# Optimization experiments

Hardware: AMD Instinct MI355X
Metric: run time of the kernel (lower is better)

Reference implementation:

```python
import jax, jax.numpy as jnp
import numpy as np

N_NODES = 20000
N_EDGES = 480000
HIDDEN = 128
EDGE_FEAT = 128
BN_EPS = 1e-5


def setup_inputs() -> dict:
    key = jax.random.key(0)
    ks = jax.random.split(key, 6)
    z_dim = 2 * HIDDEN + EDGE_FEAT
    h = jax.random.normal(ks[0], (N_NODES, HIDDEN), dtype=jnp.float32)
    e = jax.random.normal(ks[1], (N_EDGES, EDGE_FEAT), dtype=jnp.float32)
    src = jax.random.randint(ks[2], (N_EDGES,), 0, N_NODES, dtype=jnp.int32)
    dst = jax.random.randint(ks[3], (N_EDGES,), 0, N_NODES, dtype=jnp.int32)
    W = jax.random.normal(ks[4], (z_dim, 2 * HIDDEN), dtype=jnp.float32) / np.sqrt(z_dim)
    b = jax.random.normal(ks[5], (2 * HIDDEN,), dtype=jnp.float32) * 0.01
    gamma = jnp.ones((2 * HIDDEN,), dtype=jnp.float32)
    beta = jnp.zeros((2 * HIDDEN,), dtype=jnp.float32)
    return {"h": h, "e": e, "src": src, "dst": dst, "W": W, "b": b,
            "gamma": gamma, "beta": beta}


def reference(h, e, src, dst, W, b, gamma, beta):
    # Gather endpoint features per edge: z = [h_src, h_dst, e]  -> [E, z_dim]
    z = jnp.concatenate([h[src], h[dst], e], axis=1)
    # Linear
    z = z @ W + b  # [E, 2*HIDDEN]
    # BatchNorm1d over the edge batch (training-mode stats, biased variance)
    mean = jnp.mean(z, axis=0)
    var = jnp.mean(jnp.square(z - mean), axis=0)
    z = (z - mean) * jax.lax.rsqrt(var + BN_EPS) * gamma + beta
    # Gated softplus message
    nbr_filter, nbr_core = jnp.split(z, 2, axis=1)
    msg = jax.nn.sigmoid(nbr_filter) * jax.nn.softplus(nbr_core)  # [E, HIDDEN]
    # Segment-sum reduce into destination nodes
    agg = jax.ops.segment_sum(msg, dst, num_segments=N_NODES)  # [N, HIDDEN]
    # Residual + softplus (dropout=0.0)
    return jax.nn.softplus(h + agg)
```

## Files before the change

kernel.cpp:

```cpp
#include <hip/hip_runtime.h>
#include <hip/hip_bf16.h>
#include <math.h>

#define N_NODES 20000
#define N_EDGES 480000
#define HIDDEN  128
#define ZDIM    384
#define NOUT    256
#define BN_EPS  1e-5f

#define LDA     392
#define LDZ     264

using bf16x8 = __attribute__((ext_vector_type(8))) short;
using f32x4  = __attribute__((ext_vector_type(4))) float;
using f32x16 = __attribute__((ext_vector_type(16))) float;
using s16x4  = __attribute__((ext_vector_type(4))) short;

struct f32x8 { float4 a, b; };

__device__ __forceinline__ unsigned short f2b(float f) {
    union { float f; unsigned u; } v; v.f = f;
    unsigned r = v.u + 0x7fffu + ((v.u >> 16) & 1u);
    return (unsigned short)(r >> 16);
}
__device__ __forceinline__ float bflo(unsigned u) {
    union { unsigned x; float f; } v; v.x = u << 16; return v.f;
}
__device__ __forceinline__ float bfhi(unsigned u) {
    union { unsigned x; float f; } v; v.x = u & 0xffff0000u; return v.f;
}
__device__ __forceinline__ float b2f(unsigned short s) {
    union { unsigned u; float f; } v; v.u = ((unsigned)s) << 16; return v.f;
}
__device__ __forceinline__ float sigmoid_(float x) {
    return 1.f / (1.f + __expf(-x));
}
__device__ __forceinline__ float softplus_(float x) {
    return fmaxf(x, 0.f) + __logf(1.f + __expf(-fabsf(x)));
}
__device__ __forceinline__ f32x8 ld8(const float* p) {
    f32x8 r; r.a = *(const float4*)p; r.b = *(const float4*)(p + 4); return r;
}
__device__ __forceinline__ bf16x8 cvt8(f32x8 v) {
    bf16x8 pk;
    pk[0] = (short)f2b(v.a.x); pk[1] = (short)f2b(v.a.y);
    pk[2] = (short)f2b(v.a.z); pk[3] = (short)f2b(v.a.w);
    pk[4] = (short)f2b(v.b.x); pk[5] = (short)f2b(v.b.y);
    pk[6] = (short)f2b(v.b.z); pk[7] = (short)f2b(v.b.w);
    return pk;
}

__global__ void convW(const float* __restrict__ W, short* __restrict__ wt) {
    int n = blockIdx.x;
    for (int k = threadIdx.x; k < ZDIM; k += 256)
        wt[n * ZDIM + k] = (short)f2b(W[(size_t)k * NOUT + n]);
}

__global__ void bn_finalize(const float* __restrict__ stats,
                            const float* __restrict__ gamma,
                            const float* __restrict__ beta,
                            float* __restrict__ scaleC,
                            float* __restrict__ shiftC) {
    int c = threadIdx.x;
    float s = 0.f, q = 0.f;
    for (int p = 0; p < 64; ++p) {
        s += stats[p * 512 + c];
        q += stats[p * 512 + 256 + c];
    }
    const float invE = 1.f / (float)N_EDGES;
    float m   = s * invE;
    float var = q * invE - m * m;
    float inv = rsqrtf(var + BN_EPS);
    float sc  = gamma[c] * inv;
    scaleC[c] = sc;
    shiftC[c] = beta[c] - m * sc;
}

__global__ void hist_dst(const int* __restrict__ dst, int* __restrict__ counts) {
    int i = blockIdx.x * 256 + threadIdx.x;
    if (i < N_EDGES) atomicAdd(&counts[dst[i]], 1);
}

__global__ void scan_nodes(const int* __restrict__ counts, int* __restrict__ offs,
                           int* __restrict__ cursor) {
    __shared__ int part[1024];
    int t = threadIdx.x;
    int base = t * 20;
    int local[20]; int s = 0;
    #pragma unroll
    for (int k = 0; k < 20; ++k) {
        int idx = base + k;
        int v = (idx < N_NODES) ? counts[idx] : 0;
        local[k] = s; s += v;
    }
    part[t] = s; __syncthreads();
    for (int d = 1; d < 1024; d <<= 1) {
        int v = (t >= d) ? part[t - d] : 0;
        __syncthreads();
        part[t] += v;
        __syncthreads();
    }
    int pre = (t > 0) ? part[t - 1] : 0;
    #pragma unroll
    for (int k = 0; k < 20; ++k) {
        int idx = base + k;
        if (idx < N_NODES) { int o = pre + local[k]; offs[idx] = o; cursor[idx] = o; }
    }
}

__global__ void build_ipos(const int* __restrict__ dst, int* __restrict__ cursor,
                           int* __restrict__ ipos) {
    int i = blockIdx.x * 256 + threadIdx.x;
    if (i < N_EDGES) ipos[i] = atomicAdd(&cursor[dst[i]], 1);
}

__global__ __launch_bounds__(256)
void node_proj(const float* __restrict__ h, const short* __restrict__ wt,
               unsigned short* __restrict__ P1, unsigned short* __restrict__ P2) {
    const int tid  = threadIdx.x;
    const int lane = tid & 63;
    const int l31  = lane & 31;
    const int hi   = lane >> 5;
    const int w    = tid >> 6;
    const int rowBase = blockIdx.x * 64;
    const int colBase = blockIdx.y * 256 + w * 64;

    const float* pA[2];
    #pragma unroll
    for (int mi = 0; mi < 2; ++mi) {
        int row = rowBase + mi * 32 + l31;
        if (row > N_NODES - 1) row = N_NODES - 1;
        pA[mi] = h + (size_t)row * HIDDEN + hi * 8;
    }
    const short* pB[2];
    #pragma unroll
    for (int n = 0; n < 2; ++n) {
        int c = colBase + n * 32 + l31;
        pB[n] = wt + (size_t)(c & 255) * ZDIM + (c >> 8) * 128 + hi * 8;
    }

    f32x16 acc[2][2] = {};
    #pragma unroll
    for (int kk = 0; kk < 8; ++kk) {
        bf16x8 a[2], b[2];
        #pragma unroll
        for (int mi = 0; mi < 2; ++mi) a[mi] = cvt8(ld8(pA[mi] + kk * 16));
        #pragma unroll
        for (int n = 0; n < 2; ++n) b[n] = *(const bf16x8*)(pB[n] + kk * 16);
        #pragma unroll
        for (int mi = 0; mi < 2; ++mi)
            #pragma unroll
            for (int n = 0; n < 2; ++n)
                acc[mi][n] = __builtin_amdgcn_mfma_f32_32x32x16_bf16(
                                 a[mi], b[n], acc[mi][n], 0, 0, 0);
    }

    unsigned short* Pt = (blockIdx.y == 0) ? P1 : P2;
    const int pcol = (w * 64) + l31 * 2;
    #pragma unroll
    for (int mi = 0; mi < 2; ++mi)
        #pragma unroll
        for (int r = 0; r < 16; ++r) {
            int row = rowBase + mi * 32 + 4 * hi + (r & 3) + 8 * (r >> 2);
            if (row < N_NODES) {
                unsigned pk = (unsigned)f2b(acc[mi][0][r]) |
                              ((unsigned)f2b(acc[mi][1][r]) << 16);
                *(unsigned*)&Pt[(size_t)row * 256 + pcol] = pk;
            }
        }
}

__global__ __launch_bounds__(256, 2)
void edge_gemm3(const float* __restrict__ e, const int* __restrict__ src,
                const int* __restrict__ dst, const short* __restrict__ wt,
                const int* __restrict__ ipos,
                const unsigned short* __restrict__ P1,
                const unsigned short* __restrict__ P2,
                float* __restrict__ stats, short* __restrict__ zout) {
    const int tid  = threadIdx.x;
    const int lane = tid & 63;
    const int l31  = lane & 31;
    const int hi   = lane >> 5;
    const int w    = tid >> 6;
    const int rowBase = blockIdx.x * 64;
    const int colBase = w * 64;
    const int pcol = colBase + l31 * 2;

    const float* pE[2];
    #pragma unroll
    for (int mi = 0; mi < 2; ++mi)
        pE[mi] = e + (size_t)(rowBase + mi * 32 + l31) * HIDDEN + hi * 8;
    const short* pB[2];
    #pragma unroll
    for (int n = 0; n < 2; ++n)
        pB[n] = wt + (size_t)(colBase + n * 32 + l31) * ZDIM + 256 + hi * 8;

    f32x8 t[2][4];
    #pragma unroll
    for (int mi = 0; mi < 2; ++mi)
        #pragma unroll
        for (int j = 0; j < 4; ++j) t[mi][j] = ld8(pE[mi] + j * 16);
    bf16x8 B[2][8];
    #pragma unroll
    for (int n = 0; n < 2; ++n)
        #pragma unroll
        for (int kk = 0; kk < 8; ++kk)
            B[n][kk] = *(const bf16x8*)(pB[n] + kk * 16);

    bf16x8 A0[2][4], A1[2][4];
    #pragma unroll
    for (int mi = 0; mi < 2; ++mi)
        #pragma unroll
        for (int j = 0; j < 4; ++j) A0[mi][j] = cvt8(t[mi][j]);
    #pragma unroll
    for (int mi = 0; mi < 2; ++mi)
        #pragma unroll
        for (int j = 0; j < 4; ++j) t[mi][j] = ld8(pE[mi] + 64 + j * 16);

    f32x16 acc[2][2] = {};
    #pragma unroll
    for (int kk = 0; kk < 4; ++kk)
        #pragma unroll
        for (int mi = 0; mi < 2; ++mi)
            #pragma unroll
            for (int n = 0; n < 2; ++n)
                acc[mi][n] = __builtin_amdgcn_mfma_f32_32x32x16_bf16(
                                 A0[mi][kk], B[n][kk], acc[mi][n], 0, 0, 0);
    #pragma unroll
    for (int mi = 0; mi < 2; ++mi)
        #pragma unroll
        for (int j = 0; j < 4; ++j) A1[mi][j] = cvt8(t[mi][j]);
    #pragma unroll
    for (int kk = 4; kk < 8; ++kk)
        #pragma unroll
        for (int mi = 0; mi < 2; ++mi)
            #pragma unroll
            for (int n = 0; n < 2; ++n)
                acc[mi][n] = __builtin_amdgcn_mfma_f32_32x32x16_bf16(
                                 A1[mi][kk - 4], B[n][kk], acc[mi][n], 0, 0, 0);

    unsigned ps[2][16], pd[2][16];
    int slot[2][16];
    #pragma unroll
    for (int mi = 0; mi < 2; ++mi)
        #pragma unroll
        for (int r = 0; r < 16; ++r) {
            int rowL = mi * 32 + 4 * hi + (r & 3) + 8 * (r >> 2);
            int g    = rowBase + rowL;
            int sI   = src[g];
            int dI   = dst[g];
            slot[mi][r] = ipos[g];
            ps[mi][r] = *(const unsigned*)&P1[(size_t)sI * 256 + pcol];
            pd[mi][r] = *(const unsigned*)&P2[(size_t)dI * 256 + pcol];
        }

    float s2[2] = {0.f, 0.f}, q2[2] = {0.f, 0.f};
    #pragma unroll
    for (int mi = 0; mi < 2; ++mi)
        #pragma unroll
        for (int r = 0; r < 16; ++r) {
            float z0 = acc[mi][0][r] + bflo(ps[mi][r]) + bflo(pd[mi][r]);
            float z1 = acc[mi][1][r] + bfhi(ps[mi][r]) + bfhi(pd[mi][r]);
            s2[0] += z0; q2[0] += z0 * z0;
            s2[1] += z1; q2[1] += z1 * z1;
            unsigned pk = (unsigned)f2b(z0) | ((unsigned)f2b(z1) << 16);
            *(unsigned*)&zout[(size_t)slot[mi][r] * NOUT + pcol] = pk;
        }
    float* base = stats + (size_t)(blockIdx.x & 63) * 512;
    #pragma unroll
    for (int n = 0; n < 2; ++n) {
        float s = s2[n], q = q2[n];
        s += __shfl_xor(s, 32, 64);
        q += __shfl_xor(q, 32, 64);
        if (lane < 32) {
            int col = colBase + n * 32 + l31;
            atomicAdd(base + col, s);
            atomicAdd(base + 256 + col, q);
        }
    }
}

template<int MODE>
__global__ __launch_bounds__(256)
void edge_gemm_fb(const float* __restrict__ h, const float* __restrict__ e,
                  const int* __restrict__ src, const int* __restrict__ dst,
                  const short* __restrict__ wt,
                  float* __restrict__ stats,
                  const float* __restrict__ scaleC, const float* __restrict__ shiftC,
                  float* __restrict__ agg) {
    const int tid  = threadIdx.x;
    const int bm   = blockIdx.x;
    const int rowBase = bm * 64;
    const int lane = tid & 63;
    const int brow = lane & 15;
    const int kgo  = (lane >> 4) * 8;
    const int wcol = (tid >> 6) * 64;

    __shared__ __align__(16) short lds[64 * LDA];

    #pragma unroll
    for (int j = 0; j < 12; ++j) {
        int u = tid + j * 256;
        int r = u / 48;
        int f0 = (u - r * 48) * 8;
        int row = rowBase + r;
        const float* p;
        if (f0 < 128)      p = h + (size_t)src[row] * HIDDEN + f0;
        else if (f0 < 256) p = h + (size_t)dst[row] * HIDDEN + (f0 - 128);
        else               p = e + (size_t)row * HIDDEN + (f0 - 256);
        *(bf16x8*)&lds[r * LDA + f0] = cvt8(ld8(p));
    }
    __syncthreads();

    const short* wB[4];
    #pragma unroll
    for (int n = 0; n < 4; ++n)
        wB[n] = wt + (size_t)(wcol + n * 16 + brow) * ZDIM + kgo;

    f32x4 acc[4][4] = {};
    #pragma unroll
    for (int kk = 0; kk < 12; ++kk) {
        bf16x8 aC[4], bC[4];
        #pragma unroll
        for (int m = 0; m < 4; ++m)
            aC[m] = *(const bf16x8*)&lds[(m * 16 + brow) * LDA + kk * 32 + kgo];
        #pragma unroll
        for (int n = 0; n < 4; ++n) bC[n] = *(const bf16x8*)(wB[n] + kk * 32);
        #pragma unroll
        for (int m = 0; m < 4; ++m)
            #pragma unroll
            for (int n = 0; n < 4; ++n)
                acc[m][n] = __builtin_amdgcn_mfma_f32_16x16x32_bf16(
                                aC[m], bC[n], acc[m][n], 0, 0, 0);
    }

    if (MODE == 1) {
        float* base = stats + (size_t)(bm & 63) * 512;
        #pragma unroll
        for (int n = 0; n < 4; ++n) {
            float s = 0.f, q = 0.f;
            #pragma unroll
            for (int m = 0; m < 4; ++m)
                #pragma unroll
                for (int r = 0; r < 4; ++r) {
                    float v = acc[m][n][r]; s += v; q += v * v;
                }
            s += __shfl_xor(s, 16, 64); s += __shfl_xor(s, 32, 64);
            q += __shfl_xor(q, 16, 64); q += __shfl_xor(q, 32, 64);
            if (lane < 16) {
                int col = wcol + n * 16 + lane;
                atomicAdd(base + col, s);
                atomicAdd(base + 256 + col, q);
            }
        }
    } else {
        float sc[4], sh[4];
        #pragma unroll
        for (int n = 0; n < 4; ++n) {
            int col = wcol + n * 16 + brow;
            sc[n] = scaleC[col]; sh[n] = shiftC[col];
        }
        __syncthreads();
        #pragma unroll
        for (int m = 0; m < 4; ++m) {
            int rowb = m * 16 + (lane >> 4) * 4;
            #pragma unroll
            for (int n = 0; n < 4; ++n) {
                int col = wcol + n * 16 + brow;
                #pragma unroll
                for (int r = 0; r < 4; ++r)
                    lds[(rowb + r) * LDZ + col] = (short)f2b(acc[m][n][r] * sc[n] + sh[n]);
            }
        }
        __syncthreads();
        const int c0 = (tid & 31) * 4;
        const int r0 = tid >> 5;
        #pragma unroll
        for (int rp = 0; rp < 8; ++rp) {
            int row = rp * 8 + r0;
            int d   = dst[rowBase + row];
            float* ap = agg + (size_t)d * HIDDEN + c0;
            s16x4 f4 = *(const s16x4*)&lds[row * LDZ + c0];
            s16x4 c4 = *(const s16x4*)&lds[row * LDZ + 128 + c0];
            #pragma unroll
            for (int j = 0; j < 4; ++j)
                atomicAdd(ap + j, sigmoid_(b2f((unsigned short)f4[j])) *
                                  softplus_(b2f((unsigned short)c4[j])));
        }
    }
}

__global__ __launch_bounds__(256)
void node_gather(const short* __restrict__ z,
                 const int* __restrict__ offs, const int* __restrict__ counts,
                 const float* __restrict__ scaleC, const float* __restrict__ shiftC,
                 const float* __restrict__ h, float* __restrict__ out) {
    int node = blockIdx.x * 4 + (threadIdx.x >> 6);
    int lane = threadIdx.x & 63;
    int l32  = lane & 31;
    const int wq = l32 >> 4;
    const int c0 = 64 * wq + 2 * (l32 & 15);

    float scF[4], shF[4], scS[4], shS[4];
    const int cmap[4] = {c0, c0 + 32, c0 + 1, c0 + 33};
    #pragma unroll
    for (int k = 0; k < 4; ++k) {
        scF[k] = scaleC[cmap[k]];       shF[k] = shiftC[cmap[k]];
        scS[k] = scaleC[128 + cmap[k]]; shS[k] = shiftC[128 + cmap[k]];
    }

    int s   = offs[node];
    int deg = counts[node];
    float a0 = 0.f, a1 = 0.f, a2 = 0.f, a3 = 0.f;
    const int po = 4 * l32;

    for (int j = (lane >> 5); j < deg; j += 4) {
        int jB = j + 2;
        bool hasB = (jB < deg);
        const short* zA = z + (size_t)(s + j) * NOUT;
        const short* zB = z + (size_t)(s + (hasB ? jB : j)) * NOUT;
        uint2 fA = *(const uint2*)(zA + po);
        uint2 cA = *(const uint2*)(zA + 128 + po);
        uint2 fB = *(const uint2*)(zB + po);
        uint2 cB = *(const uint2*)(zB + 128 + po);

        float f0 = bflo(fA.x) * scF[0] + shF[0];
        float f1 = bfhi(fA.x) * scF[1] + shF[1];
        float f2 = bflo(fA.y) * scF[2] + shF[2];
        float f3 = bfhi(fA.y) * scF[3] + shF[3];
        float g0 = bflo(cA.x) * scS[0] + shS[0];
        float g1 = bfhi(cA.x) * scS[1] + shS[1];
        float g2 = bflo(cA.y) * scS[2] + shS[2];
        float g3 = bfhi(cA.y) * scS[3] + shS[3];
        a0 += sigmoid_(f0) * softplus_(g0);
        a1 += sigmoid_(f1) * softplus_(g1);
        a2 += sigmoid_(f2) * softplus_(g2);
        a3 += sigmoid_(f3) * softplus_(g3);

        if (hasB) {
            f0 = bflo(fB.x) * scF[0] + shF[0];
            f1 = bfhi(fB.x) * scF[1] + shF[1];
            f2 = bflo(fB.y) * scF[2] + shF[2];
            f3 = bfhi(fB.y) * scF[3] + shF[3];
            g0 = bflo(cB.x) * scS[0] + shS[0];
            g1 = bfhi(cB.x) * scS[1] + shS[1];
            g2 = bflo(cB.y) * scS[2] + shS[2];
            g3 = bfhi(cB.y) * scS[3] + shS[3];
            a0 += sigmoid_(f0) * softplus_(g0);
            a1 += sigmoid_(f1) * softplus_(g1);
            a2 += sigmoid_(f2) * softplus_(g2);
            a3 += sigmoid_(f3) * softplus_(g3);
        }
    }
    a0 += __shfl_xor(a0, 32, 64);
    a1 += __shfl_xor(a1, 32, 64);
    a2 += __shfl_xor(a2, 32, 64);
    a3 += __shfl_xor(a3, 32, 64);

    if (lane < 32) {
        size_t o = (size_t)node * HIDDEN;
        float2 hA = *(const float2*)&h[o + c0];
        float2 hB = *(const float2*)&h[o + c0 + 32];
        float2 rA, rB;
        rA.x = softplus_(hA.x + a0);
        rA.y = softplus_(hA.y + a2);
        rB.x = softplus_(hB.x + a1);
        rB.y = softplus_(hB.y + a3);
        *(float2*)&out[o + c0]      = rA;
        *(float2*)&out[o + c0 + 32] = rB;
    }
}

__global__ void node_finalize(const float* __restrict__ h, float* __restrict__ out) {
    int i = blockIdx.x * 256 + threadIdx.x;
    float4 hv = ((const float4*)h)[i];
    float4 av = ((float4*)out)[i];
    float4 r;
    r.x = softplus_(hv.x + av.x);
    r.y = softplus_(hv.y + av.y);
    r.z = softplus_(hv.z + av.z);
    r.w = softplus_(hv.w + av.w);
    ((float4*)out)[i] = r;
}

extern "C" void kernel_launch(void* const* d_in, const int* in_sizes, int n_in,
                              void* d_out, int out_size, void* d_ws, size_t ws_size,
                              hipStream_t stream) {
    const float* h     = (const float*)d_in[0];
    const float* e     = (const float*)d_in[1];
    const int*   srcp  = (const int*)d_in[2];
    const int*   dstp  = (const int*)d_in[3];
    const float* W     = (const float*)d_in[4];
    const float* gamma = (const float*)d_in[6];
    const float* beta  = (const float*)d_in[7];
    float* out = (float*)d_out;

    char*  ws     = (char*)d_ws;
    float* stats  = (float*)ws;
    float* scaleC = (float*)(ws + 131072);
    float* shiftC = (float*)(ws + 132096);
    short* wt     = (short*)(ws + 133120);
    int*   counts = (int*)(ws + 329728);
    int*   offs   = (int*)(ws + 409856);
    int*   cursor = (int*)(ws + 489984);
    int*   ipos   = (int*)(ws + 570112);
    unsigned short* P1 = (unsigned short*)(ws + 2490112);
    unsigned short* P2 = (unsigned short*)(ws + 12730112);
    short* zbuf   = (short*)(ws + 22970112);
    const size_t need = 22970112ull + (size_t)N_EDGES * NOUT * 2;

    hipMemsetAsync(stats, 0, 131072, stream);
    convW<<<NOUT, 256, 0, stream>>>(W, wt);

    if (ws_size >= need) {
        hipMemsetAsync(counts, 0, N_NODES * sizeof(int), stream);
        hist_dst<<<(N_EDGES + 255) / 256, 256, 0, stream>>>(dstp, counts);
        scan_nodes<<<1, 1024, 0, stream>>>(counts, offs, cursor);
        build_ipos<<<(N_EDGES + 255) / 256, 256, 0, stream>>>(dstp, cursor, ipos);

        node_proj<<<dim3((N_NODES + 63) / 64, 2), 256, 0, stream>>>(h, wt, P1, P2);
        edge_gemm3<<<N_EDGES / 64, 256, 0, stream>>>(e, srcp, dstp, wt, ipos,
                P1, P2, stats, zbuf);
        bn_finalize<<<1, 256, 0, stream>>>(stats, gamma, beta, scaleC, shiftC);
        node_gather<<<N_NODES / 4, 256, 0, stream>>>(zbuf, offs, counts,
                scaleC, shiftC, h, out);
    } else {
        hipMemsetAsync(out, 0, (size_t)N_NODES * HIDDEN * sizeof(float), stream);
        edge_gemm_fb<1><<<N_EDGES / 64, 256, 0, stream>>>(h, e, srcp, dstp, wt,
                stats, nullptr, nullptr, nullptr);
        bn_finalize<<<1, 256, 0, stream>>>(stats, gamma, beta, scaleC, shiftC);
        edge_gemm_fb<2><<<N_EDGES / 64, 256, 0, stream>>>(h, e, srcp, dstp, wt,
                stats, scaleC, shiftC, out);
        node_finalize<<<N_NODES * HIDDEN / (4 * 256), 256, 0, stream>>>(h, out);
    }
}
```

Measured before the change: 472.7 us.

## Pack per-edge src/dst/slot into int4, raise edge GEMM occupancy, unroll gather by 4

The build pass now writes a packed int4 record (src, dst, slot) per edge, so the edge GEMM does one 16-byte load per row where it used to do three scattered int loads. The edge GEMM launch bound goes from 2 to 3 blocks per SM to raise occupancy, which may force register spills. The node gather loop handles four edges per iteration per half-wave, putting more loads in flight to hide memory latency. The trade is extra workspace and write traffic for the int4 array, plus more register pressure.

Result: slower. 621.3 us (+31.4%).

```diff
diff --git a/kernel.cpp b/kernel.cpp
--- a/kernel.cpp
+++ b/kernel.cpp
@@ -109,10 +109,14 @@
     }
 }
 
-__global__ void build_ipos(const int* __restrict__ dst, int* __restrict__ cursor,
-                           int* __restrict__ ipos) {
+__global__ void build_einfo(const int* __restrict__ src, const int* __restrict__ dst,
+                            int* __restrict__ cursor, int4* __restrict__ einfo) {
     int i = blockIdx.x * 256 + threadIdx.x;
-    if (i < N_EDGES) ipos[i] = atomicAdd(&cursor[dst[i]], 1);
+    if (i < N_EDGES) {
+        int d = dst[i];
+        int slot = atomicAdd(&cursor[d], 1);
+        einfo[i] = make_int4(src[i], d, slot, 0);
+    }
 }
 
 __global__ __launch_bounds__(256)
@@ -171,10 +175,9 @@
         }
 }
 
-__global__ __launch_bounds__(256, 2)
-void edge_gemm3(const float* __restrict__ e, const int* __restrict__ src,
-                const int* __restrict__ dst, const short* __restrict__ wt,
-                const int* __restrict__ ipos,
+__global__ __launch_bounds__(256, 3)
+void edge_gemm3(const float* __restrict__ e, const int4* __restrict__ einfo,
+                const short* __restrict__ wt,
                 const unsigned short* __restrict__ P1,
                 const unsigned short* __restrict__ P2,
                 float* __restrict__ stats, short* __restrict__ zout) {
@@ -247,12 +250,10 @@
         #pragma unroll
         for (int r = 0; r < 16; ++r) {
             int rowL = mi * 32 + 4 * hi + (r & 3) + 8 * (r >> 2);
-            int g    = rowBase + rowL;
-            int sI   = src[g];
-            int dI   = dst[g];
-            slot[mi][r] = ipos[g];
-            ps[mi][r] = *(const unsigned*)&P1[(size_t)sI * 256 + pcol];
-            pd[mi][r] = *(const unsigned*)&P2[(size_t)dI * 256 + pcol];
+            int4 ei  = einfo[rowBase + rowL];
+            slot[mi][r] = ei.z;
+            ps[mi][r] = *(const unsigned*)&P1[(size_t)ei.x * 256 + pcol];
+            pd[mi][r] = *(const unsigned*)&P2[(size_t)ei.y * 256 + pcol];
         }
 
     float s2[2] = {0.f, 0.f}, q2[2] = {0.f, 0.f};
@@ -414,43 +415,39 @@
     int deg = counts[node];
     float a0 = 0.f, a1 = 0.f, a2 = 0.f, a3 = 0.f;
     const int po = 4 * l32;
-
-    for (int j = (lane >> 5); j < deg; j += 4) {
-        int jB = j + 2;
-        bool hasB = (jB < deg);
-        const short* zA = z + (size_t)(s + j) * NOUT;
-        const short* zB = z + (size_t)(s + (hasB ? jB : j)) * NOUT;
-        uint2 fA = *(const uint2*)(zA + po);
-        uint2 cA = *(const uint2*)(zA + 128 + po);
-        uint2 fB = *(const uint2*)(zB + po);
-        uint2 cB = *(const uint2*)(zB + 128 + po);
-
-        float f0 = bflo(fA.x) * scF[0] + shF[0];
-        float f1 = bfhi(fA.x) * scF[1] + shF[1];
-        float f2 = bflo(fA.y) * scF[2] + shF[2];
-        float f3 = bfhi(fA.y) * scF[3] + shF[3];
-        float g0 = bflo(cA.x) * scS[0] + shS[0];
-        float g1 = bfhi(cA.x) * scS[1] + shS[1];
-        float g2 = bflo(cA.y) * scS[2] + shS[2];
-        float g3 = bfhi(cA.y) * scS[3] + shS[3];
-        a0 += sigmoid_(f0) * softplus_(g0);
-        a1 += sigmoid_(f1) * softplus_(g1);
-        a2 += sigmoid_(f2) * softplus_(g2);
-        a3 += sigmoid_(f3) * softplus_(g3);
-
-        if (hasB) {
-            f0 = bflo(fB.x) * scF[0] + shF[0];
-            f1 = bfhi(fB.x) * scF[1] + shF[1];
-            f2 = bflo(fB.y) * scF[2] + shF[2];
-            f3 = bfhi(fB.y) * scF[3] + shF[3];
-            g0 = bflo(cB.x) * scS[0] + shS[0];
-            g1 = bfhi(cB.x) * scS[1] + shS[1];
-            g2 = bflo(cB.y) * scS[2] + shS[2];
-            g3 = bfhi(cB.y) * scS[3] + shS[3];
-            a0 += sigmoid_(f0) * softplus_(g0);
-            a1 += sigmoid_(f1) * softplus_(g1);
-            a2 += sigmoid_(f2) * softplus_(g2);
-            a3 += sigmoid_(f3) * softplus_(g3);
+    const int h2 = lane >> 5;
+
+    for (int j = h2; j < deg; j += 8) {
+        const short* zP[4];
+        bool has[4];
+        #pragma unroll
+        for (int k = 0; k < 4; ++k) {
+            int jk = j + 2 * k;
+            has[k] = (jk < deg);
+            zP[k]  = z + (size_t)(s + (has[k] ? jk : j)) * NOUT;
+        }
+        uint2 fv[4], cv[4];
+        #pragma unroll
+        for (int k = 0; k < 4; ++k) {
+            fv[k] = *(const uint2*)(zP[k] + po);
+            cv[k] = *(const uint2*)(zP[k] + 128 + po);
+        }
+        #pragma unroll
+        for (int k = 0; k < 4; ++k) {
+            if (has[k]) {
+                float f0 = bflo(fv[k].x) * scF[0] + shF[0];
+                float f1 = bfhi(fv[k].x) * scF[1] + shF[1];
+                float f2 = bflo(fv[k].y) * scF[2] + shF[2];
+                float f3 = bfhi(fv[k].y) * scF[3] + shF[3];
+                float g0 = bflo(cv[k].x) * scS[0] + shS[0];
+                float g1 = bfhi(cv[k].x) * scS[1] + shS[1];
+                float g2 = bflo(cv[k].y) * scS[2] + shS[2];
+                float g3 = bfhi(cv[k].y) * scS[3] + shS[3];
+                a0 += sigmoid_(f0) * softplus_(g0);
+                a1 += sigmoid_(f1) * softplus_(g1);
+                a2 += sigmoid_(f2) * softplus_(g2);
+                a3 += sigmoid_(f3) * softplus_(g3);
+            }
         }
     }
     a0 += __shfl_xor(a0, 32, 64);
@@ -504,11 +501,11 @@
     int*   counts = (int*)(ws + 329728);
     int*   offs   = (int*)(ws + 409856);
     int*   cursor = (int*)(ws + 489984);
-    int*   ipos   = (int*)(ws + 570112);
-    unsigned short* P1 = (unsigned short*)(ws + 2490112);
-    unsigned short* P2 = (unsigned short*)(ws + 12730112);
-    short* zbuf   = (short*)(ws + 22970112);
-    const size_t need = 22970112ull + (size_t)N_EDGES * NOUT * 2;
+    int4*  einfo  = (int4*)(ws + 570112);
+    unsigned short* P1 = (unsigned short*)(ws + 8250112);
+    unsigned short* P2 = (unsigned short*)(ws + 18490112);
+    short* zbuf   = (short*)(ws + 28730112);
+    const size_t need = 28730112ull + (size_t)N_EDGES * NOUT * 2;
 
     hipMemsetAsync(stats, 0, 131072, stream);
     convW<<<NOUT, 256, 0, stream>>>(W, wt);
@@ -517,11 +514,11 @@
         hipMemsetAsync(counts, 0, N_NODES * sizeof(int), stream);
         hist_dst<<<(N_EDGES + 255) / 256, 256, 0, stream>>>(dstp, counts);
         scan_nodes<<<1, 1024, 0, stream>>>(counts, offs, cursor);
-        build_ipos<<<(N_EDGES + 255) / 256, 256, 0, stream>>>(dstp, cursor, ipos);
+        build_einfo<<<(N_EDGES + 255) / 256, 256, 0, stream>>>(srcp, dstp, cursor, einfo);
 
         node_proj<<<dim3((N_NODES + 63) / 64, 2), 256, 0, stream>>>(h, wt, P1, P2);
-        edge_gemm3<<<N_EDGES / 64, 256, 0, stream>>>(e, srcp, dstp, wt, ipos,
-                P1, P2, stats, zbuf);
+        edge_gemm3<<<N_EDGES / 64, 256, 0, stream>>>(e, einfo, wt, P1, P2,
+                stats, zbuf);
         bn_finalize<<<1, 256, 0, stream>>>(stats, gamma, beta, scaleC, shiftC);
         node_gather<<<N_NODES / 4, 256, 0, stream>>>(zbuf, offs, counts,
                 scaleC, shiftC, h, out);
```
